# Performance work log

Measured on AMD Instinct MI355X. Metric: run time of the kernel, lower is better.

Reference implementation:

```python
import jax, jax.numpy as jnp
import numpy as np

ALPHA = 0.01  # ELU slope from init kwargs


def setup_inputs() -> dict:
    key = jax.random.key(0)
    k1, k2, k3, k4, k5 = jax.random.split(key, 5)
    B, L, D_IN, D_ATT = 8, 2048, 256, 128
    context = jax.random.normal(k1, (B, L, D_IN), dtype=jnp.float32)
    query = jax.random.normal(k2, (B, L, D_IN), dtype=jnp.float32)
    query_mask = jax.random.randint(k3, (B, L), 0, 2, dtype=jnp.int32)
    # Linear(in_size, attention_size, bias=False) weights (stored as [in, out])
    W_in = jax.random.normal(k4, (D_IN, D_ATT), dtype=jnp.float32) * 0.05
    W_mem = jax.random.normal(k5, (D_IN, D_ATT), dtype=jnp.float32) * 0.05
    return {"context": context, "query": query, "W_in": W_in,
            "W_mem": W_mem, "query_mask": query_mask}


def reference(context, query, W_in, W_mem, query_mask):
    # VariationalDropout is identity at inference; Linear -> ELU(alpha=0.01)
    inp = jax.nn.elu(jnp.einsum('bld,df->blf', context, W_in), ALPHA)   # [B, Lc, Datt]
    mem = jax.nn.elu(jnp.einsum('bld,df->blf', query, W_mem), ALPHA)    # [B, Lq, Datt]
    scale = inp.shape[-1] ** 0.5
    logits = jnp.einsum('bcf,bqf->bcq', inp, mem) / scale               # [B, Lc, Lq]
    big = jnp.finfo(logits.dtype).max
    # mask_diag=True: kill diagonal (self) positions
    Lq = logits.shape[-1]
    eye = jnp.eye(Lq, dtype=bool)
    logits = jnp.where(eye[None, :, :], -big, logits)
    # masked_softmax over the query axis using query_mask [B, Lq]
    valid = (query_mask > 0)[:, None, :]                                # [B, 1, Lq]
    logits = jnp.where(valid, logits, -big)
    score = jax.nn.softmax(logits, axis=-1)                             # [B, Lc, Lq]
    return jnp.einsum('bcq,bqd->bcd', score, query)                     # [B, Lc, D_in]
```

## Files before the change

kernel.cpp:

```cpp
#include <hip/hip_runtime.h>
#include <math.h>

typedef short v4s __attribute__((ext_vector_type(4)));
typedef short v8s __attribute__((ext_vector_type(8)));
typedef float v4f __attribute__((ext_vector_type(4)));

#define L2E 1.4426950408889634f
#define INV_SCALE 0.08838834764831845f
#define SCL2 (INV_SCALE * L2E)

static __device__ __forceinline__ short f2bf(float x) {
    union { float f; unsigned u; } c; c.f = x;
    unsigned u = c.u;
    unsigned r = (u + 0x7fffu + ((u >> 16) & 1u)) >> 16;
    return (short)r;
}

typedef __attribute__((address_space(3))) void lds_vt;
typedef __attribute__((address_space(1))) const void gl_vt;
static __device__ __forceinline__ void gload_lds16(const void* g, void* l) {
    __builtin_amdgcn_global_load_lds((gl_vt*)g, (lds_vt*)l, 16, 0, 0);
}

__global__ __launch_bounds__(256) void k_pre(const float* __restrict__ ctx,
                                             const float* __restrict__ qry,
                                             const float* __restrict__ Win,
                                             const float* __restrict__ Wmem,
                                             const int* __restrict__ qmask,
                                             short* __restrict__ Qa,
                                             short* __restrict__ Ka,
                                             short* __restrict__ VaT,
                                             float* __restrict__ maskadd) {
    __shared__ __align__(16) char sbuf[128 * 132 * 2];
    int x = blockIdx.x;
    int tid = threadIdx.x;
    if (x < 512) {
        short* WtS = (short*)sbuf;
        int msel = x & 255, isel = x >> 8;
        const float* X = isel ? qry : ctx;
        const float* W = isel ? Wmem : Win;
        short* Y = isel ? Ka : Qa;

        int w = tid >> 6, lane = tid & 63;
        int ln = lane & 15, qd = lane >> 4;
        int m0 = msel * 64 + w * 16;
        v4f zero = {0.f, 0.f, 0.f, 0.f};
        v4f o[8];
#pragma unroll
        for (int i = 0; i < 8; ++i) o[i] = zero;

#pragma unroll 1
        for (int kh = 0; kh < 2; ++kh) {
            if (kh) __syncthreads();
#pragma unroll 8
            for (int i = 0; i < 64; ++i) {
                int id = i * 256 + tid;
                int k = id >> 7, fp = id & 127;
                WtS[fp * 132 + k] = f2bf(W[(kh * 128 + k) * 128 + fp]);
            }
            __syncthreads();
#pragma unroll
            for (int kk = 0; kk < 4; ++kk) {
                const float* xp = X + (size_t)(m0 + ln) * 256 + kh * 128 + kk * 32 + qd * 8;
                float4 x0 = *(const float4*)xp;
                float4 x1 = *(const float4*)(xp + 4);
                v8s a;
                a[0] = f2bf(x0.x); a[1] = f2bf(x0.y); a[2] = f2bf(x0.z); a[3] = f2bf(x0.w);
                a[4] = f2bf(x1.x); a[5] = f2bf(x1.y); a[6] = f2bf(x1.z); a[7] = f2bf(x1.w);
#pragma unroll
                for (int nt = 0; nt < 8; ++nt) {
                    v8s bfr = *(const v8s*)(WtS + (nt * 16 + ln) * 132 + kk * 32 + qd * 8);
                    o[nt] = __builtin_amdgcn_mfma_f32_16x16x32_bf16(a, bfr, o[nt], 0, 0, 0);
                }
            }
        }
#pragma unroll
        for (int nt = 0; nt < 8; ++nt) {
#pragma unroll
            for (int r = 0; r < 4; ++r) {
                float v = o[nt][r];
                v = v > 0.f ? v : 0.01f * (__expf(v) - 1.f);
                Y[(size_t)(m0 + qd * 4 + r) * 128 + nt * 16 + ln] = f2bf(v);
            }
        }
    } else {
        float (*tile)[65] = (float(*)[65])sbuf;
        int t = x - 512;
        int q0 = (t & 31) * 64, d0 = ((t >> 5) & 3) * 64, b = t >> 7;
        int c = tid & 63;
        int r4 = tid >> 6;
#pragma unroll
        for (int i = 0; i < 16; ++i) {
            int r = r4 + i * 4;
            tile[r][c] = qry[(size_t)(b * 2048 + q0 + r) * 256 + d0 + c];
        }
        __syncthreads();
        int g = c >> 3, j = c & 7;
#pragma unroll
        for (int i = 0; i < 16; ++i) {
            int d = r4 + i * 4;
            int cs = ((g ^ (d & 7)) << 3) | j;
            VaT[(size_t)(b * 256 + d0 + d) * 2048 + q0 + cs] = f2bf(tile[c][d]);
        }
        if (d0 == 0 && tid < 64) {
            int qq = b * 2048 + q0 + tid;
            maskadd[qq] = (qmask[qq] > 0) ? 0.f : -__builtin_inff();
        }
    }
}

__global__ __launch_bounds__(512, 2) void k_attn(const short* __restrict__ Qa,
                                                 const short* __restrict__ Ka,
                                                 const short* __restrict__ VaT,
                                                 const float* __restrict__ maskadd,
                                                 float* __restrict__ out) {
    __shared__ __align__(16) short VaS[2][2][256 * 64];
    __shared__ __align__(16) short PS[2][64 * 64];
    __shared__ float lS[8 * 64];

    const int STEPS = 16;
    int blk = blockIdx.x;
    int b = blk & 7;
    int c0 = (blk >> 3) * 64;

    int tid = threadIdx.x;
    int w = tid >> 6, lane = tid & 63, ln = lane & 15, qd = lane >> 4;
    int g = w >> 2, wl = w & 3;
    int kv0 = g * 1024;

    const short* qbase = Qa + (size_t)(b * 2048) * 128;
    const short* kbase = Ka + (size_t)(b * 2048 + kv0 + wl * 16 + ln) * 128 + qd * 8;
    const short* vbase = VaT + (size_t)(b * 256) * 2048;
    const float* mbase = maskadd + b * 2048 + kv0 + wl * 16 + qd * 4;

    v8s qf[4][4];
#pragma unroll
    for (int ct = 0; ct < 4; ++ct) {
        const short* qp = qbase + (size_t)(c0 + ct * 16 + ln) * 128 + qd * 8;
#pragma unroll
        for (int kk = 0; kk < 4; ++kk) qf[ct][kk] = *(const v8s*)(qp + kk * 32);
    }

    v4f zero = {0.f, 0.f, 0.f, 0.f};
    v4f o[4][4];
#pragma unroll
    for (int i = 0; i < 4; ++i)
#pragma unroll
        for (int j = 0; j < 4; ++j) o[i][j] = zero;
    float lacc[4] = {0.f, 0.f, 0.f, 0.f};

    auto stageV = [&](int q0s, int buf) {
        short* base = &VaS[g][buf][0] + wl * 4096;
#pragma unroll
        for (int j = 0; j < 8; ++j) {
            int U = (wl * 8 + j) * 64 + lane;
            int d = U >> 3, cc = U & 7;
            gload_lds16(vbase + (size_t)d * 2048 + q0s + cc * 8,
                        base + j * 512);
        }
    };

    v8s kfA[4], kfB[4];
    float4 mkA, mkB;
    stageV(kv0, 0);
    asm volatile("" ::: "memory");
#pragma unroll
    for (int kk = 0; kk < 4; ++kk) kfA[kk] = *(const v8s*)(kbase + kk * 32);
    mkA = *(const float4*)(mbase);
    asm volatile("" ::: "memory");
    stageV(kv0 + 64, 1);

#define ATT_STEP(IT, KFC, MKC, KFN, MKN) do {                                  \
    int q0 = kv0 + (IT) * 64;                                                  \
    int itn = ((IT) + 1) & (STEPS - 1);                                        \
    int itn2 = ((IT) + 2) & (STEPS - 1);                                       \
    {              \
        const short* kp = kbase + (size_t)itn * 8192;                          \
        _Pragma("unroll")                                                      \
        for (int kk = 0; kk < 4; ++kk) KFN[kk] = *(const v8s*)(kp + kk * 32);  \
        MKN = *(const float4*)(mbase + itn * 64);                              \
    }                                                                          \
        \
    asm volatile("s_waitcnt vmcnt(13)" ::: "memory");                          \
    int kvb = q0 + wl * 16 + qd * 4;                                           \
    _Pragma("unroll")                                                          \
    for (int ct = 0; ct < 4; ++ct) {                                           \
        v4f s = zero;                                                          \
        _Pragma("unroll")                                                      \
        for (int kk = 0; kk < 4; ++kk)                                         \
            s = __builtin_amdgcn_mfma_f32_16x16x32_bf16(KFC[kk], qf[ct][kk],   \
                                                        s, 0, 0, 0);           \
        int cg = c0 + ct * 16 + ln;                                            \
        v4s pw;                                                                \
        float ls = 0.f;                                                        \
        _Pragma("unroll")                                                      \
        for (int r = 0; r < 4; ++r) {                                          \
            float v = s[r] * SCL2 + (&MKC.x)[r];                               \
            if (kvb + r == cg) v = -__builtin_inff();                          \
            float p = exp2f(v);                                                \
            ls += p;                                                           \
            pw[r] = f2bf(p);                                                   \
        }                                                                      \
        lacc[ct] += ls;                                                        \
        int hs = ((wl * 2 + (qd >> 1)) ^ (ln & 7));                            \
        *(v4s*)(&PS[g][0] + (ct * 16 + ln) * 64 + hs * 8 + (qd & 1) * 4) = pw; \
    }                                                                          \
    asm volatile("s_waitcnt lgkmcnt(0)" ::: "memory");                         \
    __builtin_amdgcn_s_barrier();                               \
    const short* vs = &VaS[g][(IT) & 1][0];                                    \
    __builtin_amdgcn_s_setprio(1);                                             \
    _Pragma("unroll")                                                          \
    for (int kk2 = 0; kk2 < 2; ++kk2) {                                        \
        v8s pf[4], vf[4];                                                      \
        _Pragma("unroll")                                                      \
        for (int ct = 0; ct < 4; ++ct)                                         \
            pf[ct] = *(const v8s*)(&PS[g][0] + (ct * 16 + ln) * 64 +           \
                                   (((kk2 * 4 + qd) ^ (ln & 7)) << 3));        \
        _Pragma("unroll")                                                      \
        for (int dt = 0; dt < 4; ++dt) {                                       \
            int d = wl * 64 + dt * 16 + ln;                                    \
            vf[dt] = *(const v8s*)(vs + d * 64 +                               \
                                   (((kk2 * 4 + qd) ^ (ln & 7)) << 3));        \
        }                                                                      \
        _Pragma("unroll")                                                      \
        for (int ct = 0; ct < 4; ++ct)                                         \
            _Pragma("unroll")                                                  \
            for (int dt = 0; dt < 4; ++dt)                                     \
                o[ct][dt] = __builtin_amdgcn_mfma_f32_16x16x32_bf16(           \
                    pf[ct], vf[dt], o[ct][dt], 0, 0, 0);                       \
    }                                                                          \
    __builtin_amdgcn_s_setprio(0);                                             \
            \
    asm volatile("s_waitcnt lgkmcnt(0)" ::: "memory");                         \
    stageV(kv0 + itn2 * 64, (IT) & 1);                                         \
    __builtin_amdgcn_s_barrier();                \
} while (0)

#pragma unroll 1
    for (int it2 = 0; it2 < STEPS; it2 += 2) {
        ATT_STEP(it2, kfA, mkA, kfB, mkB);
        ATT_STEP(it2 + 1, kfB, mkB, kfA, mkA);
    }
#undef ATT_STEP

    asm volatile("s_waitcnt vmcnt(0)" ::: "memory");
    __syncthreads();

#pragma unroll
    for (int ct = 0; ct < 4; ++ct) {
        float v = lacc[ct];
        v += __shfl_xor(v, 16);
        v += __shfl_xor(v, 32);
        if (qd == 0) lS[w * 64 + ct * 16 + ln] = v;
    }

    float* OS = (float*)&VaS[0][0][0];
    if (g == 1) {
#pragma unroll
        for (int ct = 0; ct < 4; ++ct)
#pragma unroll
            for (int r = 0; r < 4; ++r)
#pragma unroll
                for (int dt = 0; dt < 4; ++dt)
                    OS[(ct * 16 + qd * 4 + r) * 260 + wl * 64 + dt * 16 + ln] =
                        o[ct][dt][r];
    }
    __syncthreads();

    if (g == 0) {
#pragma unroll
        for (int ct = 0; ct < 4; ++ct) {
            float lv[4];
#pragma unroll
            for (int r = 0; r < 4; ++r) {
                float s = 0.f;
#pragma unroll
                for (int wv = 0; wv < 8; ++wv)
                    s += lS[wv * 64 + ct * 16 + qd * 4 + r];
                lv[r] = s;
            }
            int rowg = b * 2048 + c0 + ct * 16 + qd * 4;
#pragma unroll
            for (int r = 0; r < 4; ++r) {
                float inv = 1.f / lv[r];
#pragma unroll
                for (int dt = 0; dt < 4; ++dt) {
                    int col = wl * 64 + dt * 16 + ln;
                    float sum = o[ct][dt][r] +
                                OS[(ct * 16 + qd * 4 + r) * 260 + col];
                    out[(size_t)(rowg + r) * 256 + col] = sum * inv;
                }
            }
        }
    }
}

extern "C" void kernel_launch(void* const* d_in, const int* in_sizes, int n_in,
                              void* d_out, int out_size, void* d_ws, size_t ws_size,
                              hipStream_t stream) {
    const float* ctx  = (const float*)d_in[0];
    const float* qry  = (const float*)d_in[1];
    const float* win  = (const float*)d_in[2];
    const float* wmem = (const float*)d_in[3];
    const int* qmask  = (const int*)d_in[4];
    float* out = (float*)d_out;

    char* ws = (char*)d_ws;
    short* Qa      = (short*)(ws);
    short* Ka      = (short*)(ws + (4u << 20));
    short* VaT     = (short*)(ws + (8u << 20));
    float* maskadd = (float*)(ws + (16u << 20));

    k_pre<<<dim3(1536), 256, 0, stream>>>(ctx, qry, win, wmem, qmask,
                                          Qa, Ka, VaT, maskadd);
    k_attn<<<dim3(256), 512, 0, stream>>>(Qa, Ka, VaT, maskadd, out);
}
```

Baseline: 151.1 us.

## Fuse V transpose into projection kernel and restructure attention without P staging

```diff
diff --git a/kernel.cpp b/kernel.cpp
--- a/kernel.cpp
+++ b/kernel.cpp
@@ -14,6 +14,14 @@
     unsigned u = c.u;
     unsigned r = (u + 0x7fffu + ((u >> 16) & 1u)) >> 16;
     return (short)r;
+}
+
+static __device__ __forceinline__ v4f mfma16(v4s a, v4s b, v4f c) {
+#if __has_builtin(__builtin_amdgcn_mfma_f32_16x16x16_bf16)
+    return __builtin_amdgcn_mfma_f32_16x16x16_bf16(a, b, c, 0, 0, 0);
+#else
+    return __builtin_amdgcn_mfma_f32_16x16x16bf16_1k(a, b, c, 0, 0, 0);
+#endif
 }
 
 typedef __attribute__((address_space(3))) void lds_vt;
@@ -31,79 +39,75 @@
                                              short* __restrict__ Ka,
                                              short* __restrict__ VaT,
                                              float* __restrict__ maskadd) {
-    __shared__ __align__(16) char sbuf[128 * 132 * 2];
+    __shared__ __align__(16) short WtS[128 * 132];
+    __shared__ __align__(16) short Tt[256 * 72];
     int x = blockIdx.x;
     int tid = threadIdx.x;
-    if (x < 512) {
-        short* WtS = (short*)sbuf;
-        int msel = x & 255, isel = x >> 8;
-        const float* X = isel ? qry : ctx;
-        const float* W = isel ? Wmem : Win;
-        short* Y = isel ? Ka : Qa;
-
-        int w = tid >> 6, lane = tid & 63;
-        int ln = lane & 15, qd = lane >> 4;
-        int m0 = msel * 64 + w * 16;
-        v4f zero = {0.f, 0.f, 0.f, 0.f};
-        v4f o[8];
-#pragma unroll
-        for (int i = 0; i < 8; ++i) o[i] = zero;
+    int msel = x & 255, isel = x >> 8;
+    const float* X = isel ? qry : ctx;
+    const float* W = isel ? Wmem : Win;
+    short* Y = isel ? Ka : Qa;
+
+    int w = tid >> 6, lane = tid & 63;
+    int ln = lane & 15, qd = lane >> 4;
+    int m0 = msel * 64 + w * 16;
+    v4f zero = {0.f, 0.f, 0.f, 0.f};
+    v4f o[8];
+#pragma unroll
+    for (int i = 0; i < 8; ++i) o[i] = zero;
 
 #pragma unroll 1
-        for (int kh = 0; kh < 2; ++kh) {
-            if (kh) __syncthreads();
+    for (int kh = 0; kh < 2; ++kh) {
+        if (kh) __syncthreads();
 #pragma unroll 8
-            for (int i = 0; i < 64; ++i) {
-                int id = i * 256 + tid;
-                int k = id >> 7, fp = id & 127;
-                WtS[fp * 132 + k] = f2bf(W[(kh * 128 + k) * 128 + fp]);
-            }
-            __syncthreads();
-#pragma unroll
-            for (int kk = 0; kk < 4; ++kk) {
-                const float* xp = X + (size_t)(m0 + ln) * 256 + kh * 128 + kk * 32 + qd * 8;
-                float4 x0 = *(const float4*)xp;
-                float4 x1 = *(const float4*)(xp + 4);
-                v8s a;
-                a[0] = f2bf(x0.x); a[1] = f2bf(x0.y); a[2] = f2bf(x0.z); a[3] = f2bf(x0.w);
-                a[4] = f2bf(x1.x); a[5] = f2bf(x1.y); a[6] = f2bf(x1.z); a[7] = f2bf(x1.w);
-#pragma unroll
-                for (int nt = 0; nt < 8; ++nt) {
-                    v8s bfr = *(const v8s*)(WtS + (nt * 16 + ln) * 132 + kk * 32 + qd * 8);
-                    o[nt] = __builtin_amdgcn_mfma_f32_16x16x32_bf16(a, bfr, o[nt], 0, 0, 0);
-                }
-            }
-        }
-#pragma unroll
-        for (int nt = 0; nt < 8; ++nt) {
-#pragma unroll
-            for (int r = 0; r < 4; ++r) {
-                float v = o[nt][r];
-                v = v > 0.f ? v : 0.01f * (__expf(v) - 1.f);
-                Y[(size_t)(m0 + qd * 4 + r) * 128 + nt * 16 + ln] = f2bf(v);
-            }
-        }
-    } else {
-        float (*tile)[65] = (float(*)[65])sbuf;
-        int t = x - 512;
-        int q0 = (t & 31) * 64, d0 = ((t >> 5) & 3) * 64, b = t >> 7;
-        int c = tid & 63;
-        int r4 = tid >> 6;
-#pragma unroll
-        for (int i = 0; i < 16; ++i) {
-            int r = r4 + i * 4;
-            tile[r][c] = qry[(size_t)(b * 2048 + q0 + r) * 256 + d0 + c];
+        for (int i = 0; i < 64; ++i) {
+            int id = i * 256 + tid;
+            int k = id >> 7, fp = id & 127;
+            WtS[fp * 132 + k] = f2bf(W[(kh * 128 + k) * 128 + fp]);
         }
         __syncthreads();
-        int g = c >> 3, j = c & 7;
-#pragma unroll
-        for (int i = 0; i < 16; ++i) {
-            int d = r4 + i * 4;
-            int cs = ((g ^ (d & 7)) << 3) | j;
-            VaT[(size_t)(b * 256 + d0 + d) * 2048 + q0 + cs] = f2bf(tile[c][d]);
-        }
-        if (d0 == 0 && tid < 64) {
-            int qq = b * 2048 + q0 + tid;
+#pragma unroll
+        for (int kk = 0; kk < 4; ++kk) {
+            const float* xp = X + (size_t)(m0 + ln) * 256 + kh * 128 + kk * 32 + qd * 8;
+            float4 x0 = *(const float4*)xp;
+            float4 x1 = *(const float4*)(xp + 4);
+            v8s a;
+            a[0] = f2bf(x0.x); a[1] = f2bf(x0.y); a[2] = f2bf(x0.z); a[3] = f2bf(x0.w);
+            a[4] = f2bf(x1.x); a[5] = f2bf(x1.y); a[6] = f2bf(x1.z); a[7] = f2bf(x1.w);
+            if (isel) {
+#pragma unroll
+                for (int si = 0; si < 8; ++si)
+                    Tt[(kh * 128 + kk * 32 + qd * 8 + si) * 72 + (w * 16 + ln)] = a[si];
+            }
+#pragma unroll
+            for (int nt = 0; nt < 8; ++nt) {
+                v8s bfr = *(const v8s*)(WtS + (nt * 16 + ln) * 132 + kk * 32 + qd * 8);
+                o[nt] = __builtin_amdgcn_mfma_f32_16x16x32_bf16(a, bfr, o[nt], 0, 0, 0);
+            }
+        }
+    }
+#pragma unroll
+    for (int nt = 0; nt < 8; ++nt) {
+#pragma unroll
+        for (int r = 0; r < 4; ++r) {
+            float v = o[nt][r];
+            v = v > 0.f ? v : 0.01f * (__expf(v) - 1.f);
+            Y[(size_t)(m0 + qd * 4 + r) * 128 + nt * 16 + ln] = f2bf(v);
+        }
+    }
+
+    if (isel) {
+        __syncthreads();
+        int b2 = msel >> 5, q0 = (msel & 31) * 64;
+        int dr = tid >> 3, j = tid & 7;
+#pragma unroll
+        for (int i = 0; i < 8; ++i) {
+            int d = dr + i * 32;
+            v8s vv = *(const v8s*)(Tt + d * 72 + j * 8);
+            *(v8s*)(VaT + ((size_t)(b2 * 256 + d)) * 2048 + q0 + j * 8) = vv;
+        }
+        if (tid < 64) {
+            int qq = b2 * 2048 + q0 + tid;
             maskadd[qq] = (qmask[qq] > 0) ? 0.f : -__builtin_inff();
         }
     }
@@ -115,180 +119,129 @@
                                                  const float* __restrict__ maskadd,
                                                  float* __restrict__ out) {
     __shared__ __align__(16) short VaS[2][2][256 * 64];
-    __shared__ __align__(16) short PS[2][64 * 64];
-    __shared__ float lS[8 * 64];
-
-    const int STEPS = 16;
+    __shared__ float lS[256];
+
     int blk = blockIdx.x;
     int b = blk & 7;
     int c0 = (blk >> 3) * 64;
 
     int tid = threadIdx.x;
     int w = tid >> 6, lane = tid & 63, ln = lane & 15, qd = lane >> 4;
-    int g = w >> 2, wl = w & 3;
+    int g = w >> 2, wl = w & 3, cw = (w >> 1) & 1, dv = w & 1;
     int kv0 = g * 1024;
 
-    const short* qbase = Qa + (size_t)(b * 2048) * 128;
-    const short* kbase = Ka + (size_t)(b * 2048 + kv0 + wl * 16 + ln) * 128 + qd * 8;
-    const short* vbase = VaT + (size_t)(b * 256) * 2048;
-    const float* mbase = maskadd + b * 2048 + kv0 + wl * 16 + qd * 4;
-
-    v8s qf[4][4];
-#pragma unroll
-    for (int ct = 0; ct < 4; ++ct) {
-        const short* qp = qbase + (size_t)(c0 + ct * 16 + ln) * 128 + qd * 8;
+    const short* kbase = Ka + ((size_t)(b * 2048 + kv0 + ln)) * 128 + qd * 8;
+    const short* vbase = VaT + (size_t)b * 256 * 2048;
+    const float* mbase = maskadd + b * 2048 + kv0 + qd * 4;
+
+    v8s qf[2][4];
+#pragma unroll
+    for (int ct = 0; ct < 2; ++ct) {
+        const short* qp = Qa + ((size_t)(b * 2048 + c0 + cw * 32 + ct * 16 + ln)) * 128 + qd * 8;
 #pragma unroll
         for (int kk = 0; kk < 4; ++kk) qf[ct][kk] = *(const v8s*)(qp + kk * 32);
     }
 
     v4f zero = {0.f, 0.f, 0.f, 0.f};
-    v4f o[4][4];
-#pragma unroll
-    for (int i = 0; i < 4; ++i)
-#pragma unroll
-        for (int j = 0; j < 4; ++j) o[i][j] = zero;
-    float lacc[4] = {0.f, 0.f, 0.f, 0.f};
+    v4f o[2][8];
+#pragma unroll
+    for (int i = 0; i < 2; ++i)
+#pragma unroll
+        for (int j = 0; j < 8; ++j) o[i][j] = zero;
+    float lacc[2] = {0.f, 0.f};
 
     auto stageV = [&](int q0s, int buf) {
-        short* base = &VaS[g][buf][0] + wl * 4096;
+        short* ldsb = &VaS[g][buf][0];
 #pragma unroll
         for (int j = 0; j < 8; ++j) {
-            int U = (wl * 8 + j) * 64 + lane;
-            int d = U >> 3, cc = U & 7;
-            gload_lds16(vbase + (size_t)d * 2048 + q0s + cc * 8,
-                        base + j * 512);
+            int U = j * 256 + wl * 64 + lane;
+            int d = U >> 3, u = U & 7;
+            gload_lds16(vbase + (size_t)d * 2048 + q0s + ((u ^ (d & 7)) << 3),
+                        ldsb + (size_t)(j * 256 + wl * 64) * 8);
         }
     };
 
-    v8s kfA[4], kfB[4];
-    float4 mkA, mkB;
     stageV(kv0, 0);
-    asm volatile("" ::: "memory");
-#pragma unroll
-    for (int kk = 0; kk < 4; ++kk) kfA[kk] = *(const v8s*)(kbase + kk * 32);
-    mkA = *(const float4*)(mbase);
-    asm volatile("" ::: "memory");
-    stageV(kv0 + 64, 1);
-
-#define ATT_STEP(IT, KFC, MKC, KFN, MKN) do {                                  \
-    int q0 = kv0 + (IT) * 64;                                                  \
-    int itn = ((IT) + 1) & (STEPS - 1);                                        \
-    int itn2 = ((IT) + 2) & (STEPS - 1);                                       \
-    {              \
-        const short* kp = kbase + (size_t)itn * 8192;                          \
-        _Pragma("unroll")                                                      \
-        for (int kk = 0; kk < 4; ++kk) KFN[kk] = *(const v8s*)(kp + kk * 32);  \
-        MKN = *(const float4*)(mbase + itn * 64);                              \
-    }                                                                          \
-        \
-    asm volatile("s_waitcnt vmcnt(13)" ::: "memory");                          \
-    int kvb = q0 + wl * 16 + qd * 4;                                           \
-    _Pragma("unroll")                                                          \
-    for (int ct = 0; ct < 4; ++ct) {                                           \
-        v4f s = zero;                                                          \
-        _Pragma("unroll")                                                      \
-        for (int kk = 0; kk < 4; ++kk)                                         \
-            s = __builtin_amdgcn_mfma_f32_16x16x32_bf16(KFC[kk], qf[ct][kk],   \
-                                                        s, 0, 0, 0);           \
-        int cg = c0 + ct * 16 + ln;                                            \
-        v4s pw;                                                                \
-        float ls = 0.f;                                                        \
-        _Pragma("unroll")                                                      \
-        for (int r = 0; r < 4; ++r) {                                          \
-            float v = s[r] * SCL2 + (&MKC.x)[r];                               \
-            if (kvb + r == cg) v = -__builtin_inff();                          \
-            float p = exp2f(v);                                                \
-            ls += p;                                                           \
-            pw[r] = f2bf(p);                                                   \
-        }                                                                      \
-        lacc[ct] += ls;                                                        \
-        int hs = ((wl * 2 + (qd >> 1)) ^ (ln & 7));                            \
-        *(v4s*)(&PS[g][0] + (ct * 16 + ln) * 64 + hs * 8 + (qd & 1) * 4) = pw; \
-    }                                                                          \
-    asm volatile("s_waitcnt lgkmcnt(0)" ::: "memory");                         \
-    __builtin_amdgcn_s_barrier();                               \
-    const short* vs = &VaS[g][(IT) & 1][0];                                    \
-    __builtin_amdgcn_s_setprio(1);                                             \
-    _Pragma("unroll")                                                          \
-    for (int kk2 = 0; kk2 < 2; ++kk2) {                                        \
-        v8s pf[4], vf[4];                                                      \
-        _Pragma("unroll")                                                      \
-        for (int ct = 0; ct < 4; ++ct)                                         \
-            pf[ct] = *(const v8s*)(&PS[g][0] + (ct * 16 + ln) * 64 +           \
-                                   (((kk2 * 4 + qd) ^ (ln & 7)) << 3));        \
-        _Pragma("unroll")                                                      \
-        for (int dt = 0; dt < 4; ++dt) {                                       \
-            int d = wl * 64 + dt * 16 + ln;                                    \
-            vf[dt] = *(const v8s*)(vs + d * 64 +                               \
-                                   (((kk2 * 4 + qd) ^ (ln & 7)) << 3));        \
-        }                                                                      \
-        _Pragma("unroll")                                                      \
-        for (int ct = 0; ct < 4; ++ct)                                         \
-            _Pragma("unroll")                                                  \
-            for (int dt = 0; dt < 4; ++dt)                                     \
-                o[ct][dt] = __builtin_amdgcn_mfma_f32_16x16x32_bf16(           \
-                    pf[ct], vf[dt], o[ct][dt], 0, 0, 0);                       \
-    }                                                                          \
-    __builtin_amdgcn_s_setprio(0);                                             \
-            \
-    asm volatile("s_waitcnt lgkmcnt(0)" ::: "memory");                         \
-    stageV(kv0 + itn2 * 64, (IT) & 1);                                         \
-    __builtin_amdgcn_s_barrier();                \
-} while (0)
-
-#pragma unroll 1
-    for (int it2 = 0; it2 < STEPS; it2 += 2) {
-        ATT_STEP(it2, kfA, mkA, kfB, mkB);
-        ATT_STEP(it2 + 1, kfB, mkB, kfA, mkA);
-    }
-#undef ATT_STEP
-
     asm volatile("s_waitcnt vmcnt(0)" ::: "memory");
     __syncthreads();
 
-#pragma unroll
-    for (int ct = 0; ct < 4; ++ct) {
-        float v = lacc[ct];
-        v += __shfl_xor(v, 16);
-        v += __shfl_xor(v, 32);
-        if (qd == 0) lS[w * 64 + ct * 16 + ln] = v;
-    }
+#pragma unroll 1
+    for (int t = 0; t < 16; ++t) {
+        stageV(kv0 + ((t + 1) & 15) * 64, (t & 1) ^ 1);
+        const short* vs = &VaS[g][t & 1][0];
+        const short* kt = kbase + (size_t)t * 8192;
+        const float* mt = mbase + t * 64;
+#pragma unroll
+        for (int s = 0; s < 4; ++s) {
+            v8s kf[4];
+#pragma unroll
+            for (int kk = 0; kk < 4; ++kk)
+                kf[kk] = *(const v8s*)(kt + s * 2048 + kk * 32);
+            float4 mk = *(const float4*)(mt + s * 16);
+            v4s pw[2];
+#pragma unroll
+            for (int ct = 0; ct < 2; ++ct) {
+                v4f sa = zero;
+#pragma unroll
+                for (int kk = 0; kk < 4; ++kk)
+                    sa = __builtin_amdgcn_mfma_f32_16x16x32_bf16(kf[kk], qf[ct][kk], sa, 0, 0, 0);
+                int cg = c0 + cw * 32 + ct * 16 + ln;
+                int kvg = kv0 + t * 64 + s * 16 + qd * 4;
+#pragma unroll
+                for (int r = 0; r < 4; ++r) {
+                    float v = sa[r] * SCL2 + (&mk.x)[r];
+                    if (kvg + r == cg) v = -__builtin_inff();
+                    float p = exp2f(v);
+                    lacc[ct] += p;
+                    pw[ct][r] = f2bf(p);
+                }
+            }
+#pragma unroll
+            for (int dt = 0; dt < 8; ++dt) {
+                int d = dv * 128 + dt * 16 + ln;
+                v4s vf = *(const v4s*)(vs + d * 64 +
+                          (((s * 2 + (qd >> 1)) ^ (d & 7)) << 3) + ((qd & 1) << 2));
+                o[0][dt] = mfma16(pw[0], vf, o[0][dt]);
+                o[1][dt] = mfma16(pw[1], vf, o[1][dt]);
+            }
+        }
+        asm volatile("s_waitcnt vmcnt(0)" ::: "memory");
+        __builtin_amdgcn_s_barrier();
+    }
+
+    float lv0 = lacc[0], lv1 = lacc[1];
+    lv0 += __shfl_xor(lv0, 16); lv0 += __shfl_xor(lv0, 32);
+    lv1 += __shfl_xor(lv1, 16); lv1 += __shfl_xor(lv1, 32);
+    if (lane < 16) { lS[w * 32 + ln] = lv0; lS[w * 32 + 16 + ln] = lv1; }
+    __syncthreads();
 
     float* OS = (float*)&VaS[0][0][0];
     if (g == 1) {
 #pragma unroll
-        for (int ct = 0; ct < 4; ++ct)
+        for (int ct = 0; ct < 2; ++ct) {
+            int cl = cw * 32 + ct * 16 + qd * 4;
 #pragma unroll
             for (int r = 0; r < 4; ++r)
 #pragma unroll
-                for (int dt = 0; dt < 4; ++dt)
-                    OS[(ct * 16 + qd * 4 + r) * 260 + wl * 64 + dt * 16 + ln] =
-                        o[ct][dt][r];
+                for (int dt = 0; dt < 8; ++dt)
+                    OS[(cl + r) * 260 + dv * 128 + dt * 16 + ln] = o[ct][dt][r];
+        }
     }
     __syncthreads();
-
     if (g == 0) {
 #pragma unroll
-        for (int ct = 0; ct < 4; ++ct) {
-            float lv[4];
+        for (int ct = 0; ct < 2; ++ct) {
+            int cl = cw * 32 + ct * 16 + qd * 4;
 #pragma unroll
             for (int r = 0; r < 4; ++r) {
-                float s = 0.f;
-#pragma unroll
-                for (int wv = 0; wv < 8; ++wv)
-                    s += lS[wv * 64 + ct * 16 + qd * 4 + r];
-                lv[r] = s;
-            }
-            int rowg = b * 2048 + c0 + ct * 16 + qd * 4;
-#pragma unroll
-            for (int r = 0; r < 4; ++r) {
-                float inv = 1.f / lv[r];
-#pragma unroll
-                for (int dt = 0; dt < 4; ++dt) {
-                    int col = wl * 64 + dt * 16 + ln;
-                    float sum = o[ct][dt][r] +
-                                OS[(ct * 16 + qd * 4 + r) * 260 + col];
-                    out[(size_t)(rowg + r) * 256 + col] = sum * inv;
+                float ltot = lS[w * 32 + ct * 16 + qd * 4 + r]
+                           + lS[(w + 4) * 32 + ct * 16 + qd * 4 + r];
+                float inv = 1.f / ltot;
+                size_t rowg = (size_t)(b * 2048 + c0 + cl + r);
+#pragma unroll
+                for (int dt = 0; dt < 8; ++dt) {
+                    int col = dv * 128 + dt * 16 + ln;
+                    out[rowg * 256 + col] = (o[ct][dt][r] + OS[(cl + r) * 260 + col]) * inv;
                 }
             }
         }
@@ -311,7 +264,7 @@
     short* VaT     = (short*)(ws + (8u << 20));
     float* maskadd = (float*)(ws + (16u << 20));
 
-    k_pre<<<dim3(1536), 256, 0, stream>>>(ctx, qry, win, wmem, qmask,
-                                          Qa, Ka, VaT, maskadd);
+    k_pre<<<dim3(512), 256, 0, stream>>>(ctx, qry, win, wmem, qmask,
+                                         Qa, Ka, VaT, maskadd);
     k_attn<<<dim3(256), 512, 0, stream>>>(Qa, Ka, VaT, maskadd, out);
 }
```

After: 181.7 us. 20.2% more time.
